# Optimization experiments

Hardware: AMD Instinct MI355X
Metric: run time of the kernel (lower is better)

Reference implementation:

```python
import jax, jax.numpy as jnp
import numpy as np

B, S, H, NH, FF, L, BLK, R = 2, 4096, 768, 12, 3072, 4, 64, 3
NB = S // BLK          # 64 blocks
D = H // NH            # 64 per-head dim
A = 3 + 2 + R          # window(3) + global(2) + random(R) attended blocks
EPS = 1e-12
SCALE = 1.0 / np.sqrt(D).astype(np.float32)


def setup_inputs() -> dict:
    key = jax.random.key(0)
    ks = jax.random.split(key, 12)
    p = lambda k, shp: jax.random.normal(k, shp, jnp.float32) * 0.02
    return {
        "input_ids": jax.random.normal(ks[0], (B, S, 4), jnp.float32),
        "rand_blocks": jax.random.randint(ks[1], (NB, R), 0, NB, jnp.int32),
        "emb_w": p(ks[2], (4, H)), "emb_b": jnp.zeros((H,), jnp.float32),
        "ln1_g": jnp.ones((L, H), jnp.float32), "ln1_b": jnp.zeros((L, H), jnp.float32),
        "wq": p(ks[3], (L, H, H)), "bq": jnp.zeros((L, H), jnp.float32),
        "wk": p(ks[4], (L, H, H)), "bk": jnp.zeros((L, H), jnp.float32),
        "wv": p(ks[5], (L, H, H)), "bv": jnp.zeros((L, H), jnp.float32),
        "wo": p(ks[6], (L, H, H)), "bo": jnp.zeros((L, H), jnp.float32),
        "ln2_g": jnp.ones((L, H), jnp.float32), "ln2_b": jnp.zeros((L, H), jnp.float32),
        "w1": p(ks[7], (L, H, FF)), "b1": jnp.zeros((L, FF), jnp.float32),
        "w2": p(ks[8], (L, FF, H)), "b2": jnp.zeros((L, H), jnp.float32),
        "clf_w": p(ks[9], (H, 4)), "clf_b": jnp.zeros((4,), jnp.float32),
    }


def _ln(x, g, b):
    m = x.mean(-1, keepdims=True)
    v = jnp.var(x, axis=-1, keepdims=True)  # biased var, like torch LayerNorm
    return (x - m) * jax.lax.rsqrt(v + EPS) * g + b


def _attend_idx(rand_blocks):
    # per query block: [i-1, i, i+1] window (edge-clamped), global {0, NB-1}, R random
    ar = jnp.arange(NB)
    win = jnp.stack([jnp.clip(ar - 1, 0, NB - 1), ar, jnp.clip(ar + 1, 0, NB - 1)], 1)
    glb = jnp.broadcast_to(jnp.array([0, NB - 1], jnp.int32), (NB, 2))
    return jnp.concatenate([win.astype(jnp.int32), glb, rand_blocks], 1)  # [NB, A]


def _attn(x, wq, bq, wk, bk, wv, bv, wo, bo, idx):
    def heads(t):  # [B,S,H] -> [B,NH,NB,BLK,D]
        return t.reshape(B, NB, BLK, NH, D).transpose(0, 3, 1, 2, 4)
    q = heads(x @ wq + bq)
    k = heads(x @ wk + bk)
    v = heads(x @ wv + bv)
    kg = k[:, :, idx].reshape(B, NH, NB, A * BLK, D)  # gather attended key blocks
    vg = v[:, :, idx].reshape(B, NH, NB, A * BLK, D)
    s = jnp.einsum('bhnqd,bhnkd->bhnqk', q, kg) * SCALE  # [B,NH,NB,BLK,A*BLK]
    p = jax.nn.softmax(s, axis=-1)
    o = jnp.einsum('bhnqk,bhnkd->bhnqd', p, vg)
    o = o.transpose(0, 2, 3, 1, 4).reshape(B, S, H)
    return o @ wo + bo


def reference(input_ids, rand_blocks, emb_w, emb_b, ln1_g, ln1_b, wq, bq, wk, bk,
              wv, bv, wo, bo, ln2_g, ln2_b, w1, b1, w2, b2, clf_w, clf_b):
    idx = _attend_idx(rand_blocks)
    x = input_ids @ emb_w + emb_b
    for l in range(L):
        h = _ln(x, ln1_g[l], ln1_b[l])
        x = x + _attn(h, wq[l], bq[l], wk[l], bk[l], wv[l], bv[l], wo[l], bo[l], idx)
        h = _ln(x, ln2_g[l], ln2_b[l])
        x = x + (jax.nn.gelu(h @ w1[l] + b1[l], approximate=False) @ w2[l] + b2[l])
    logits = x @ clf_w + clf_b
    return jax.nn.softmax(logits, axis=-1)
```

## Files before the change

kernel.cpp:

```cpp
#include <hip/hip_runtime.h>
#include <math.h>

constexpr int B  = 2;
constexpr int S  = 4096;
constexpr int H  = 768;
constexpr int NH = 12;
constexpr int FF = 3072;
constexpr int L  = 4;
constexpr int R  = 3;
constexpr int NB = 64;
constexpr int AB = 8;
constexpr float SCALE = 0.125f;
constexpr int QKV_N = 3 * H;

constexpr int ROWS = B * S;
constexpr size_t XSZ = (size_t)B * S * H;

typedef short bf16x8 __attribute__((ext_vector_type(8)));
typedef unsigned short u16x8 __attribute__((ext_vector_type(8)));
typedef unsigned short u16x4 __attribute__((ext_vector_type(4)));
typedef float f32x4 __attribute__((ext_vector_type(4)));
typedef unsigned short ushort_t;

__device__ __forceinline__ ushort_t f2b(float f) {
  union { float f; unsigned u; } c; c.f = f;
  unsigned r = c.u + 0x7fffu + ((c.u >> 16) & 1u);
  return (ushort_t)(r >> 16);
}

__device__ __forceinline__ float gelu_f(float x) {
  float y = 0.7978845608f * x * (1.0f + 0.044715f * x * x);
  float e = __expf(2.0f * y);
  float th = 1.0f - 2.0f / (e + 1.0f);
  return 0.5f * x * (1.0f + th);
}

__device__ __forceinline__ void gload16(const void* g, void* l) {
  __builtin_amdgcn_global_load_lds(
      (const __attribute__((address_space(1))) unsigned int*)g,
      (__attribute__((address_space(3))) unsigned int*)l, 16, 0, 0);
}

__global__ __launch_bounds__(256) void embed_kernel(
    const float* __restrict__ ids, const float* __restrict__ w,
    const float* __restrict__ bvec, float* __restrict__ x) {
  int i = blockIdx.x * 256 + threadIdx.x;
  if (i >= (int)XSZ) return;
  int hc = i % H;
  int bs = i / H;
  float s = bvec[hc];
  #pragma unroll
  for (int j = 0; j < 4; ++j) s += ids[bs * 4 + j] * w[j * H + hc];
  x[i] = s;
}

__global__ __launch_bounds__(256) void ln_kernel(
    const float* __restrict__ x, const float* __restrict__ g,
    const float* __restrict__ bvec, ushort_t* __restrict__ out) {
  int row = blockIdx.x;
  const float* xr = x + (size_t)row * H;
  int t = threadIdx.x;
  float v0 = xr[t], v1 = xr[t + 256], v2 = xr[t + 512];
  float s  = v0 + v1 + v2;
  float ss = v0 * v0 + v1 * v1 + v2 * v2;
  for (int off = 1; off < 64; off <<= 1) {
    s  += __shfl_xor(s,  off);
    ss += __shfl_xor(ss, off);
  }
  __shared__ float sm[8];
  int w = t >> 6, lane = t & 63;
  if (lane == 0) { sm[w] = s; sm[4 + w] = ss; }
  __syncthreads();
  s  = sm[0] + sm[1] + sm[2] + sm[3];
  ss = sm[4] + sm[5] + sm[6] + sm[7];
  float mean = s * (1.0f / H);
  float var  = ss * (1.0f / H) - mean * mean;
  float rstd = rsqrtf(var + 1e-12f);
  ushort_t* orow = out + (size_t)row * H;
  orow[t]       = f2b((v0 - mean) * rstd * g[t]       + bvec[t]);
  orow[t + 256] = f2b((v1 - mean) * rstd * g[t + 256] + bvec[t + 256]);
  orow[t + 512] = f2b((v2 - mean) * rstd * g[t + 512] + bvec[t + 512]);
}

__global__ __launch_bounds__(256) void tcvt_kernel(
    const float* __restrict__ in, ushort_t* __restrict__ out,
    int K, int N, size_t inZ, size_t outZ) {
  __shared__ float tile[32][33];
  const float* inz = in + blockIdx.z * inZ;
  ushort_t* outz = out + blockIdx.z * outZ;
  int k0 = blockIdx.y * 32, n0 = blockIdx.x * 32;
  int tx = threadIdx.x & 31, ty = threadIdx.x >> 5;
  #pragma unroll
  for (int i = 0; i < 4; ++i) {
    int kk = ty + i * 8;
    tile[kk][tx] = inz[(size_t)(k0 + kk) * N + n0 + tx];
  }
  __syncthreads();
  #pragma unroll
  for (int i = 0; i < 4; ++i) {
    int nn = ty + i * 8;
    outz[(size_t)(n0 + nn) * K + k0 + tx] = f2b(tile[tx][nn]);
  }
}

__global__ __launch_bounds__(256) void concat_bias_kernel(
    const float* __restrict__ bq, const float* __restrict__ bk,
    const float* __restrict__ bv, float* __restrict__ out) {
  int i = blockIdx.x * 256 + threadIdx.x;
  if (i >= L * QKV_N) return;
  int l = i / QKV_N, c = i % QKV_N;
  float val = (c < H) ? bq[l * H + c] : (c < 2 * H) ? bk[l * H + c - H] : bv[l * H + c - 2 * H];
  out[i] = val;
}

template <int BN, int EPI>
__global__ __launch_bounds__(256, (BN == 256 ? 2 : 3)) void bgemm(
    const ushort_t* __restrict__ A, const ushort_t* __restrict__ Wt,
    const float* __restrict__ bias, const float* __restrict__ res,
    float* __restrict__ Cf, ushort_t* __restrict__ Cb, ushort_t* __restrict__ Cv,
    int M, int N, int K, int ncol) {
  constexpr int LDSB = (128 + BN) * 32;
  constexpr int NLD  = (128 + BN) / 64;
  constexpr int NI   = BN / 32;
  __shared__ ushort_t lds[3 * LDSB];

  const int nwg = (int)gridDim.x;
  const int qq = nwg >> 3, r0 = nwg & 7;
  const int xcd = (int)blockIdx.x & 7, loc = (int)blockIdx.x >> 3;
  const int swz = (xcd < r0 ? xcd * (qq + 1) : r0 * (qq + 1) + (xcd - r0) * qq) + loc;
  const int bm = (swz / ncol) * 128, bn = (swz % ncol) * BN;

  const int t = threadIdx.x;
  const int wid = t >> 6, lane = t & 63;
  const int fcol = lane & 15, fgrp = lane >> 4;
  const int wm = wid >> 1, wn = wid & 1;

  const ushort_t* src[NLD];
  int dst[NLD];
  #pragma unroll
  for (int j = 0; j < NLD; ++j) {
    int idx = j * 2048 + t * 8;
    dst[j] = idx;
    int ch = (idx >> 3) & 3;
    int row;
    const ushort_t* base;
    if (idx < 4096) { row = idx >> 5;           base = A  + (size_t)(bm + row) * K; }
    else            { row = (idx - 4096) >> 5;  base = Wt + (size_t)(bn + row) * K; }
    src[j] = base + ((ch ^ ((row >> 1) & 3)) << 3);
  }

  f32x4 acc[4][NI] = {};

  #pragma unroll
  for (int j = 0; j < NLD; ++j) gload16(src[j], &lds[dst[j]]);
  #pragma unroll
  for (int j = 0; j < NLD; ++j) gload16(src[j] + 32, &lds[LDSB + dst[j]]);
  int kgl = 64;

  int bo0 = 0, bo1 = LDSB, bo2 = 2 * LDSB;
  const int NT = K >> 5;
  for (int tau = 0; tau < NT; ++tau) {
    if (tau + 2 < NT) {
      #pragma unroll
      for (int j = 0; j < NLD; ++j) gload16(src[j] + kgl, &lds[bo2 + dst[j]]);
      kgl += 32;
      if constexpr (BN == 256) { asm volatile("s_waitcnt vmcnt(12)" ::: "memory"); }
      else                     { asm volatile("s_waitcnt vmcnt(8)"  ::: "memory"); }
    } else if (tau + 2 == NT) {
      if constexpr (BN == 256) { asm volatile("s_waitcnt vmcnt(6)" ::: "memory"); }
      else                     { asm volatile("s_waitcnt vmcnt(4)" ::: "memory"); }
    } else {
      asm volatile("s_waitcnt vmcnt(0)" ::: "memory");
    }
    __builtin_amdgcn_sched_barrier(0);
    __builtin_amdgcn_s_barrier();
    __builtin_amdgcn_sched_barrier(0);

    bf16x8 af[4], bfr[NI];
    #pragma unroll
    for (int mi = 0; mi < 4; ++mi) {
      int row = wm * 64 + mi * 16 + fcol;
      af[mi] = *(const bf16x8*)&lds[bo0 + row * 32 + ((fgrp ^ ((row >> 1) & 3)) << 3)];
    }
    #pragma unroll
    for (int ni = 0; ni < NI; ++ni) {
      int row = wn * (BN / 2) + ni * 16 + fcol;
      bfr[ni] = *(const bf16x8*)&lds[bo0 + 4096 + row * 32 + ((fgrp ^ ((row >> 1) & 3)) << 3)];
    }
    __builtin_amdgcn_s_setprio(1);
    #pragma unroll
    for (int mi = 0; mi < 4; ++mi)
      #pragma unroll
      for (int ni = 0; ni < NI; ++ni)
        acc[mi][ni] = __builtin_amdgcn_mfma_f32_16x16x32_bf16(af[mi], bfr[ni], acc[mi][ni], 0, 0, 0);
    __builtin_amdgcn_s_setprio(0);

    if (tau < NT - 1) {
      __builtin_amdgcn_sched_barrier(0);
      __builtin_amdgcn_s_barrier();
      __builtin_amdgcn_sched_barrier(0);
    }
    int tmp = bo0; bo0 = bo1; bo1 = bo2; bo2 = tmp;
  }

  if (EPI == 0 && bn >= 2 * H) {
    #pragma unroll
    for (int mi = 0; mi < 4; ++mi) {
      const int m = bm + wm * 64 + mi * 16 + fgrp * 4;
      #pragma unroll
      for (int ni = 0; ni < NI; ++ni) {
        const int n = bn + wn * (BN / 2) + ni * 16 + fcol;
        const float bb = bias[n];
        u16x4 pk;
        #pragma unroll
        for (int r = 0; r < 4; ++r) pk[r] = f2b(acc[mi][ni][r] + bb);
        *(u16x4*)&Cv[(size_t)(n - 2 * H) * M + m] = pk;
      }
    }
    return;
  }
  #pragma unroll
  for (int mi = 0; mi < 4; ++mi) {
    const int m = bm + wm * 64 + mi * 16 + fgrp * 4;
    #pragma unroll
    for (int ni = 0; ni < NI; ++ni) {
      const int n = bn + wn * (BN / 2) + ni * 16 + fcol;
      const float bb = bias[n];
      #pragma unroll
      for (int r = 0; r < 4; ++r) {
        float val = acc[mi][ni][r] + bb;
        if (EPI == 1) {
          Cf[(size_t)(m + r) * N + n] = val + res[(size_t)(m + r) * N + n];
        } else if (EPI == 2) {
          Cb[(size_t)(m + r) * N + n] = f2b(gelu_f(val));
        } else {
          Cb[(size_t)(m + r) * N + n] = f2b(val);
        }
      }
    }
  }
}

__global__ __launch_bounds__(256) void attn_mfma(
    const ushort_t* __restrict__ qkv, const ushort_t* __restrict__ vT,
    const int* __restrict__ rb, ushort_t* __restrict__ ao) {
  __shared__ ushort_t Ks[2][64 * 72];
  __shared__ ushort_t Vt[2][64 * 72];
  __shared__ ushort_t Ps[4][16 * 72];
  const int n = blockIdx.x, hh = blockIdx.y, b = blockIdx.z;
  const int t = threadIdx.x;
  const int wid = t >> 6, lane = t & 63;
  const int fcol = lane & 15, fgrp = lane >> 4;
  const int qr0 = n * 64 + wid * 16;

  bf16x8 qf[2];
  #pragma unroll
  for (int kc = 0; kc < 2; ++kc)
    qf[kc] = *(const bf16x8*)&qkv[((size_t)(b * S) + qr0 + fcol) * QKV_N + hh * 64 + kc * 32 + fgrp * 8];

  f32x4 oacc[4] = {};
  float mrow[4], lrow[4];
  #pragma unroll
  for (int r = 0; r < 4; ++r) { mrow[r] = -1e30f; lrow[r] = 0.f; }

  int kbs[AB];
  kbs[0] = (n > 0) ? n - 1 : 0;
  kbs[1] = n;
  kbs[2] = (n < NB - 1) ? n + 1 : NB - 1;
  kbs[3] = 0;
  kbs[4] = NB - 1;
  kbs[5] = rb[n * R + 0];
  kbs[6] = rb[n * R + 1];
  kbs[7] = rb[n * R + 2];

  const ushort_t* kbase = qkv + (size_t)(b * S) * QKV_N + H + hh * 64;
  const ushort_t* vbase = vT + (size_t)(hh * 64) * ROWS + b * S;

  const int srow = t >> 3;
  const int soff = (t & 7) * 8;

  {
    const int kb = kbs[0];
    u16x8 k0 = *(const u16x8*)&kbase[(size_t)(kb * 64 + srow) * QKV_N + soff];
    u16x8 k1 = *(const u16x8*)&kbase[(size_t)(kb * 64 + srow + 32) * QKV_N + soff];
    u16x8 v0 = *(const u16x8*)&vbase[(size_t)srow * ROWS + kb * 64 + soff];
    u16x8 v1 = *(const u16x8*)&vbase[(size_t)(srow + 32) * ROWS + kb * 64 + soff];
    *(u16x8*)&Ks[0][srow * 72 + soff]        = k0;
    *(u16x8*)&Ks[0][(srow + 32) * 72 + soff] = k1;
    *(u16x8*)&Vt[0][srow * 72 + soff]        = v0;
    *(u16x8*)&Vt[0][(srow + 32) * 72 + soff] = v1;
  }
  __syncthreads();

  for (int a = 0; a < AB; ++a) {
    const int buf = a & 1;

    u16x8 pk0, pk1, pv0, pv1;
    if (a + 1 < AB) {
      const int kb = kbs[a + 1];
      pk0 = *(const u16x8*)&kbase[(size_t)(kb * 64 + srow) * QKV_N + soff];
      pk1 = *(const u16x8*)&kbase[(size_t)(kb * 64 + srow + 32) * QKV_N + soff];
      pv0 = *(const u16x8*)&vbase[(size_t)srow * ROWS + kb * 64 + soff];
      pv1 = *(const u16x8*)&vbase[(size_t)(srow + 32) * ROWS + kb * 64 + soff];
    }

    f32x4 sacc[4] = {};
    __builtin_amdgcn_s_setprio(1);
    #pragma unroll
    for (int ni = 0; ni < 4; ++ni)
      #pragma unroll
      for (int kc = 0; kc < 2; ++kc) {
        bf16x8 kf = *(const bf16x8*)&Ks[buf][(ni * 16 + fcol) * 72 + kc * 32 + fgrp * 8];
        sacc[ni] = __builtin_amdgcn_mfma_f32_16x16x32_bf16(qf[kc], kf, sacc[ni], 0, 0, 0);
      }
    __builtin_amdgcn_s_setprio(0);

    #pragma unroll
    for (int ni = 0; ni < 4; ++ni)
      #pragma unroll
      for (int r = 0; r < 4; ++r) sacc[ni][r] *= SCALE;
    #pragma unroll
    for (int r = 0; r < 4; ++r) {
      float tm = fmaxf(fmaxf(sacc[0][r], sacc[1][r]), fmaxf(sacc[2][r], sacc[3][r]));
      tm = fmaxf(tm, __shfl_xor(tm, 1));
      tm = fmaxf(tm, __shfl_xor(tm, 2));
      tm = fmaxf(tm, __shfl_xor(tm, 4));
      tm = fmaxf(tm, __shfl_xor(tm, 8));
      float mn = fmaxf(mrow[r], tm);
      float corr = __expf(mrow[r] - mn);
      mrow[r] = mn;
      float rs = 0.f;
      #pragma unroll
      for (int ni = 0; ni < 4; ++ni) {
        float p = __expf(sacc[ni][r] - mn);
        sacc[ni][r] = p;
        rs += p;
      }
      rs += __shfl_xor(rs, 1);
      rs += __shfl_xor(rs, 2);
      rs += __shfl_xor(rs, 4);
      rs += __shfl_xor(rs, 8);
      lrow[r] = lrow[r] * corr + rs;
      #pragma unroll
      for (int ni = 0; ni < 4; ++ni) oacc[ni][r] *= corr;
    }

    if (a + 1 < AB) {
      *(u16x8*)&Ks[buf ^ 1][srow * 72 + soff]        = pk0;
      *(u16x8*)&Ks[buf ^ 1][(srow + 32) * 72 + soff] = pk1;
      *(u16x8*)&Vt[buf ^ 1][srow * 72 + soff]        = pv0;
      *(u16x8*)&Vt[buf ^ 1][(srow + 32) * 72 + soff] = pv1;
    }

    #pragma unroll
    for (int ni = 0; ni < 4; ++ni)
      #pragma unroll
      for (int r = 0; r < 4; ++r)
        Ps[wid][(fgrp * 4 + r) * 72 + ni * 16 + fcol] = f2b(sacc[ni][r]);

    bf16x8 pa[2];
    #pragma unroll
    for (int kc = 0; kc < 2; ++kc)
      pa[kc] = *(const bf16x8*)&Ps[wid][fcol * 72 + kc * 32 + fgrp * 8];

    __builtin_amdgcn_s_setprio(1);
    #pragma unroll
    for (int kc = 0; kc < 2; ++kc)
      #pragma unroll
      for (int ni = 0; ni < 4; ++ni) {
        bf16x8 vb = *(const bf16x8*)&Vt[buf][(ni * 16 + fcol) * 72 + kc * 32 + fgrp * 8];
        oacc[ni] = __builtin_amdgcn_mfma_f32_16x16x32_bf16(pa[kc], vb, oacc[ni], 0, 0, 0);
      }
    __builtin_amdgcn_s_setprio(0);

    __syncthreads();
  }

  #pragma unroll
  for (int r = 0; r < 4; ++r) {
    float inv = 1.0f / lrow[r];
    int row = qr0 + fgrp * 4 + r;
    #pragma unroll
    for (int ni = 0; ni < 4; ++ni)
      ao[((size_t)(b * S) + row) * H + hh * 64 + ni * 16 + fcol] = f2b(oacc[ni][r] * inv);
  }
}

__global__ __launch_bounds__(64) void clf_kernel(
    const float* __restrict__ x, const float* __restrict__ w,
    const float* __restrict__ bvec, float* __restrict__ out) {
  int row = blockIdx.x;
  int lane = threadIdx.x;
  const float* xr = x + (size_t)row * H;
  float p0 = 0.f, p1 = 0.f, p2 = 0.f, p3 = 0.f;
  for (int d = lane; d < H; d += 64) {
    float xv = xr[d];
    p0 += xv * w[d * 4 + 0];
    p1 += xv * w[d * 4 + 1];
    p2 += xv * w[d * 4 + 2];
    p3 += xv * w[d * 4 + 3];
  }
  for (int off = 1; off < 64; off <<= 1) {
    p0 += __shfl_xor(p0, off);
    p1 += __shfl_xor(p1, off);
    p2 += __shfl_xor(p2, off);
    p3 += __shfl_xor(p3, off);
  }
  if (lane == 0) {
    float l0 = p0 + bvec[0], l1 = p1 + bvec[1], l2 = p2 + bvec[2], l3 = p3 + bvec[3];
    float mx = fmaxf(fmaxf(l0, l1), fmaxf(l2, l3));
    float e0 = __expf(l0 - mx), e1 = __expf(l1 - mx), e2 = __expf(l2 - mx), e3 = __expf(l3 - mx);
    float inv = 1.0f / (e0 + e1 + e2 + e3);
    out[row * 4 + 0] = e0 * inv;
    out[row * 4 + 1] = e1 * inv;
    out[row * 4 + 2] = e2 * inv;
    out[row * 4 + 3] = e3 * inv;
  }
}

extern "C" void kernel_launch(void* const* d_in, const int* in_sizes, int n_in,
                              void* d_out, int out_size, void* d_ws, size_t ws_size,
                              hipStream_t stream) {
  const float* input_ids = (const float*)d_in[0];
  const int*   rand_bl   = (const int*)  d_in[1];
  const float* emb_w = (const float*)d_in[2];
  const float* emb_b = (const float*)d_in[3];
  const float* ln1_g = (const float*)d_in[4];
  const float* ln1_b = (const float*)d_in[5];
  const float* wq = (const float*)d_in[6];
  const float* bq = (const float*)d_in[7];
  const float* wk = (const float*)d_in[8];
  const float* bk = (const float*)d_in[9];
  const float* wv = (const float*)d_in[10];
  const float* bv = (const float*)d_in[11];
  const float* wo = (const float*)d_in[12];
  const float* bo = (const float*)d_in[13];
  const float* ln2_g = (const float*)d_in[14];
  const float* ln2_b = (const float*)d_in[15];
  const float* w1 = (const float*)d_in[16];
  const float* b1 = (const float*)d_in[17];
  const float* w2 = (const float*)d_in[18];
  const float* b2 = (const float*)d_in[19];
  const float* clf_w = (const float*)d_in[20];
  const float* clf_b = (const float*)d_in[21];

  char* p = (char*)d_ws;
  float*    x    = (float*)p;    p += XSZ * 4;
  ushort_t* h    = (ushort_t*)p; p += XSZ * 2;
  ushort_t* qkv  = (ushort_t*)p; p += (size_t)ROWS * QKV_N * 2;
  ushort_t* ao   = (ushort_t*)p; p += XSZ * 2;
  ushort_t* ff   = qkv;
  ushort_t* vT   = (ushort_t*)p; p += (size_t)H * ROWS * 2;
  ushort_t* qkvT = (ushort_t*)p; p += (size_t)L * QKV_N * H * 2;
  ushort_t* woT  = (ushort_t*)p; p += (size_t)L * H * H * 2;
  ushort_t* w1T  = (ushort_t*)p; p += (size_t)L * H * FF * 2;
  ushort_t* w2T  = (ushort_t*)p; p += (size_t)L * FF * H * 2;
  float*    bqkv = (float*)p;    p += (size_t)L * QKV_N * 4;

  tcvt_kernel<<<dim3(H / 32, H / 32, L), 256, 0, stream>>>(
      wq, qkvT + 0 * H * H, H, H, (size_t)H * H, (size_t)QKV_N * H);
  tcvt_kernel<<<dim3(H / 32, H / 32, L), 256, 0, stream>>>(
      wk, qkvT + 1 * H * H, H, H, (size_t)H * H, (size_t)QKV_N * H);
  tcvt_kernel<<<dim3(H / 32, H / 32, L), 256, 0, stream>>>(
      wv, qkvT + 2 * H * H, H, H, (size_t)H * H, (size_t)QKV_N * H);
  tcvt_kernel<<<dim3(H / 32, H / 32, L), 256, 0, stream>>>(
      wo, woT, H, H, (size_t)H * H, (size_t)H * H);
  tcvt_kernel<<<dim3(FF / 32, H / 32, L), 256, 0, stream>>>(
      w1, w1T, H, FF, (size_t)H * FF, (size_t)H * FF);
  tcvt_kernel<<<dim3(H / 32, FF / 32, L), 256, 0, stream>>>(
      w2, w2T, FF, H, (size_t)FF * H, (size_t)FF * H);
  concat_bias_kernel<<<(L * QKV_N + 255) / 256, 256, 0, stream>>>(bq, bk, bv, bqkv);

  embed_kernel<<<(int)((XSZ + 255) / 256), 256, 0, stream>>>(input_ids, emb_w, emb_b, x);

  for (int l = 0; l < L; ++l) {
    ln_kernel<<<ROWS, 256, 0, stream>>>(x, ln1_g + l * H, ln1_b + l * H, h);

    bgemm<256, 0><<<(ROWS / 128) * (QKV_N / 256), 256, 0, stream>>>(
        h, qkvT + (size_t)l * QKV_N * H, bqkv + l * QKV_N, nullptr,
        nullptr, qkv, vT, ROWS, QKV_N, H, QKV_N / 256);

    attn_mfma<<<dim3(NB, NH, B), 256, 0, stream>>>(qkv, vT, rand_bl, ao);

    bgemm<128, 1><<<(ROWS / 128) * (H / 128), 256, 0, stream>>>(
        ao, woT + (size_t)l * H * H, bo + l * H, x, x, nullptr, nullptr, ROWS, H, H, H / 128);

    ln_kernel<<<ROWS, 256, 0, stream>>>(x, ln2_g + l * H, ln2_b + l * H, h);

    bgemm<256, 2><<<(ROWS / 128) * (FF / 256), 256, 0, stream>>>(
        h, w1T + (size_t)l * H * FF, b1 + l * FF, nullptr,
        nullptr, ff, nullptr, ROWS, FF, H, FF / 256);

    bgemm<128, 1><<<(ROWS / 128) * (H / 128), 256, 0, stream>>>(
        ff, w2T + (size_t)l * FF * H, b2 + l * H, x, x, nullptr, nullptr, ROWS, H, FF, H / 128);
  }

  clf_kernel<<<ROWS, 64, 0, stream>>>(x, clf_w, clf_b, (float*)d_out);
}
```

Before: 1.012 ms.

## Use one barrier per GEMM k-step and unroll triple-buffer rotation by three

The GEMM main loop now waits on vmcnt and hits a single barrier at the top of each k-step. Only then does it issue the global-to-LDS prefetch into the buffer that was read in the previous step, which removes the second per-iteration barrier. The loop is unrolled by three so buffer offsets are compile-time constants, and the swizzled LDS fragment offsets are precomputed once. This assumes the number of k-tiles is a multiple of three and gives the prefetch slightly less lead time, since it is issued after the barrier.

```diff
diff --git a/kernel.cpp b/kernel.cpp
--- a/kernel.cpp
+++ b/kernel.cpp
@@ -39,6 +39,13 @@
   __builtin_amdgcn_global_load_lds(
       (const __attribute__((address_space(1))) unsigned int*)g,
       (__attribute__((address_space(3))) unsigned int*)l, 16, 0, 0);
+}
+
+template <int N>
+__device__ __forceinline__ void waitvm() {
+  if constexpr (N == 0)      { asm volatile("s_waitcnt vmcnt(0)" ::: "memory"); }
+  else if constexpr (N == 4) { asm volatile("s_waitcnt vmcnt(4)" ::: "memory"); }
+  else                       { asm volatile("s_waitcnt vmcnt(6)" ::: "memory"); }
 }
 
 __global__ __launch_bounds__(256) void embed_kernel(
@@ -149,6 +156,18 @@
     src[j] = base + ((ch ^ ((row >> 1) & 3)) << 3);
   }
 
+  int aoff[4], boff[NI];
+  #pragma unroll
+  for (int mi = 0; mi < 4; ++mi) {
+    int row = wm * 64 + mi * 16 + fcol;
+    aoff[mi] = row * 32 + ((fgrp ^ ((row >> 1) & 3)) << 3);
+  }
+  #pragma unroll
+  for (int ni = 0; ni < NI; ++ni) {
+    int row = wn * (BN / 2) + ni * 16 + fcol;
+    boff[ni] = 4096 + row * 32 + ((fgrp ^ ((row >> 1) & 3)) << 3);
+  }
+
   f32x4 acc[4][NI] = {};
 
   #pragma unroll
@@ -157,51 +176,45 @@
   for (int j = 0; j < NLD; ++j) gload16(src[j] + 32, &lds[LDSB + dst[j]]);
   int kgl = 64;
 
-  int bo0 = 0, bo1 = LDSB, bo2 = 2 * LDSB;
+#define GEMM_STEP(P, DOSTAGE, WN)                                          \
+  {                                                                        \
+    waitvm<WN>();                                                          \
+    __builtin_amdgcn_sched_barrier(0);                                     \
+    __builtin_amdgcn_s_barrier();                                          \
+    __builtin_amdgcn_sched_barrier(0);                                     \
+    if (DOSTAGE) {                                                         \
+      _Pragma("unroll")                                                    \
+      for (int j = 0; j < NLD; ++j)                                        \
+        gload16(src[j] + kgl, &lds[(((P) + 2) % 3) * LDSB + dst[j]]);      \
+      kgl += 32;                                                           \
+    }                                                                      \
+    bf16x8 af[4], bfr[NI];                                                 \
+    _Pragma("unroll")                                                      \
+    for (int mi = 0; mi < 4; ++mi)                                         \
+      af[mi] = *(const bf16x8*)&lds[(P) * LDSB + aoff[mi]];                \
+    _Pragma("unroll")                                                      \
+    for (int ni = 0; ni < NI; ++ni)                                        \
+      bfr[ni] = *(const bf16x8*)&lds[(P) * LDSB + boff[ni]];               \
+    __builtin_amdgcn_s_setprio(1);                                         \
+    _Pragma("unroll")                                                      \
+    for (int mi = 0; mi < 4; ++mi)                                         \
+      _Pragma("unroll")                                                    \
+      for (int ni = 0; ni < NI; ++ni)                                      \
+        acc[mi][ni] = __builtin_amdgcn_mfma_f32_16x16x32_bf16(             \
+            af[mi], bfr[ni], acc[mi][ni], 0, 0, 0);                        \
+    __builtin_amdgcn_s_setprio(0);                                         \
+  }
+
   const int NT = K >> 5;
-  for (int tau = 0; tau < NT; ++tau) {
-    if (tau + 2 < NT) {
-      #pragma unroll
-      for (int j = 0; j < NLD; ++j) gload16(src[j] + kgl, &lds[bo2 + dst[j]]);
-      kgl += 32;
-      if constexpr (BN == 256) { asm volatile("s_waitcnt vmcnt(12)" ::: "memory"); }
-      else                     { asm volatile("s_waitcnt vmcnt(8)"  ::: "memory"); }
-    } else if (tau + 2 == NT) {
-      if constexpr (BN == 256) { asm volatile("s_waitcnt vmcnt(6)" ::: "memory"); }
-      else                     { asm volatile("s_waitcnt vmcnt(4)" ::: "memory"); }
-    } else {
-      asm volatile("s_waitcnt vmcnt(0)" ::: "memory");
-    }
-    __builtin_amdgcn_sched_barrier(0);
-    __builtin_amdgcn_s_barrier();
-    __builtin_amdgcn_sched_barrier(0);
-
-    bf16x8 af[4], bfr[NI];
-    #pragma unroll
-    for (int mi = 0; mi < 4; ++mi) {
-      int row = wm * 64 + mi * 16 + fcol;
-      af[mi] = *(const bf16x8*)&lds[bo0 + row * 32 + ((fgrp ^ ((row >> 1) & 3)) << 3)];
-    }
-    #pragma unroll
-    for (int ni = 0; ni < NI; ++ni) {
-      int row = wn * (BN / 2) + ni * 16 + fcol;
-      bfr[ni] = *(const bf16x8*)&lds[bo0 + 4096 + row * 32 + ((fgrp ^ ((row >> 1) & 3)) << 3)];
-    }
-    __builtin_amdgcn_s_setprio(1);
-    #pragma unroll
-    for (int mi = 0; mi < 4; ++mi)
-      #pragma unroll
-      for (int ni = 0; ni < NI; ++ni)
-        acc[mi][ni] = __builtin_amdgcn_mfma_f32_16x16x32_bf16(af[mi], bfr[ni], acc[mi][ni], 0, 0, 0);
-    __builtin_amdgcn_s_setprio(0);
-
-    if (tau < NT - 1) {
-      __builtin_amdgcn_sched_barrier(0);
-      __builtin_amdgcn_s_barrier();
-      __builtin_amdgcn_sched_barrier(0);
-    }
-    int tmp = bo0; bo0 = bo1; bo1 = bo2; bo2 = tmp;
-  }
+  for (int tau = 0; tau < NT - 3; tau += 3) {
+    GEMM_STEP(0, true, NLD)
+    GEMM_STEP(1, true, NLD)
+    GEMM_STEP(2, true, NLD)
+  }
+  GEMM_STEP(0, true,  NLD)
+  GEMM_STEP(1, false, NLD)
+  GEMM_STEP(2, false, 0)
+#undef GEMM_STEP
 
   if (EPI == 0 && bn >= 2 * H) {
     #pragma unroll
```

Measured after the change: 1.004 ms. About the same (-0.8%).
